# Kernel optimization log

Measured on AMD Instinct MI355X. Metric: run time of the kernel, lower is better.

## Reference

```python
import jax, jax.numpy as jnp
import numpy as np

N = 100000
E = 800000
IN_FEATS = 128
H_FEATS = 128
HEADS = 4
OUT = H_FEATS // HEADS  # 32
NEG_SLOPE = 0.2  # DGL GATConv default


def gat_conv(x, src, dst, W, attn_l, attn_r, bias):
    """DGL-style GATConv. x: [N, F_in] -> [N, HEADS, OUT]."""
    h = (x @ W).reshape(N, HEADS, OUT)                      # projected features
    el = jnp.sum(h * attn_l, axis=-1)                       # [N, H]
    er = jnp.sum(h * attn_r, axis=-1)                       # [N, H]
    e = jax.nn.leaky_relu(el[src] + er[dst], NEG_SLOPE)     # [E, H] edge logits
    # edge softmax over incoming edges of each dst node
    m = jax.ops.segment_max(e, dst, num_segments=N)          # [N, H]
    ex = jnp.exp(e - m[dst])                                 # [E, H]
    s = jax.ops.segment_sum(ex, dst, num_segments=N)         # [N, H]
    a = ex / s[dst]                                          # [E, H]
    msg = h[src] * a[:, :, None]                             # [E, H, OUT]
    out = jax.ops.segment_sum(msg, dst, num_segments=N)      # [N, H, OUT]
    return out + bias.reshape(1, HEADS, OUT)


def setup_inputs() -> dict:
    key = jax.random.key(0)
    ks = jax.random.split(key, 12)
    feat = jax.random.normal(ks[0], (N, IN_FEATS), dtype=jnp.float32)
    src = jax.random.randint(ks[1], (E,), 0, N)
    dst = jax.random.randint(ks[2], (E,), 0, N)
    s1 = 1.0 / np.sqrt(IN_FEATS)
    s2 = 1.0 / np.sqrt(H_FEATS)
    return {
        "feat": feat,
        "src": src,
        "dst": dst,
        "W1": jax.random.normal(ks[3], (IN_FEATS, HEADS * OUT), dtype=jnp.float32) * s1,
        "al1": jax.random.normal(ks[4], (HEADS, OUT), dtype=jnp.float32) * s2,
        "ar1": jax.random.normal(ks[5], (HEADS, OUT), dtype=jnp.float32) * s2,
        "b1": jnp.zeros((HEADS * OUT,), dtype=jnp.float32),
        "W2": jax.random.normal(ks[6], (H_FEATS, HEADS * OUT), dtype=jnp.float32) * s2,
        "al2": jax.random.normal(ks[7], (HEADS, OUT), dtype=jnp.float32) * s2,
        "ar2": jax.random.normal(ks[8], (HEADS, OUT), dtype=jnp.float32) * s2,
        "b2": jnp.zeros((HEADS * OUT,), dtype=jnp.float32),
    }


def reference(feat, src, dst, W1, al1, ar1, b1, W2, al2, ar2, b2):
    h = gat_conv(feat, src, dst, W1, al1, ar1, b1).reshape(N, H_FEATS)  # flatten(1)
    h = jax.nn.relu(h)
    h = gat_conv(h, src, dst, W2, al2, ar2, b2).mean(axis=1)            # mean over heads
    return h
```

## Files before the change

### kernel.cpp

```cpp
#include <hip/hip_runtime.h>
#include <math.h>

#define N_NODES 100000
#define N_EDGES 800000
#define NEG_SLOPE 0.2f

typedef __attribute__((ext_vector_type(8))) short short8;
typedef __attribute__((ext_vector_type(4))) float floatx4;

__device__ __forceinline__ float lrelu(float x) { return x > 0.f ? x : NEG_SLOPE * x; }

__device__ __forceinline__ unsigned bf16_rne(float f) {
    unsigned u = __float_as_uint(f);
    return (u + 0x7fffu + ((u >> 16) & 1u)) >> 16;
}
__device__ __forceinline__ unsigned bfpack(float lo, float hi) {
    return bf16_rne(lo) | (bf16_rne(hi) << 16);
}
__device__ __forceinline__ float bflo(unsigned p) { return __uint_as_float(p << 16); }
__device__ __forceinline__ float bfhi(unsigned p) { return __uint_as_float(p & 0xffff0000u); }

__global__ __launch_bounds__(256) void k_hist_wprep(const int* __restrict__ dst,
                                                    int* __restrict__ deg,
                                                    const float* __restrict__ W1,
                                                    const float* __restrict__ W2,
                                                    unsigned short* __restrict__ wt1,
                                                    unsigned short* __restrict__ wt2) {
    int b = blockIdx.x;
    if (b < 3125) {
        int e = b * 256 + threadIdx.x;
        if (e < N_EDGES) atomicAdd(&deg[dst[e]], 1);
    } else {
        int tid = (b - 3125) * 256 + threadIdx.x;
        const float* W = (tid < 16384) ? W1 : W2;
        unsigned short* wt = (tid < 16384) ? wt1 : wt2;
        int t = tid & 16383;
        int n = t >> 7, k = t & 127;
        wt[t] = (unsigned short)bf16_rne(W[k * 128 + n]);
    }
}

__global__ __launch_bounds__(256) void k_scan(const int* __restrict__ deg,
                                              int* __restrict__ rs,
                                              int* __restrict__ cursor,
                                              int* __restrict__ bsums,
                                              int* __restrict__ done) {
    __shared__ int sd[256];
    int tid = threadIdx.x, b = blockIdx.x;
    int base = b * 1024 + tid * 4;
    int v0 = (base + 0 < N_NODES) ? deg[base + 0] : 0;
    int v1 = (base + 1 < N_NODES) ? deg[base + 1] : 0;
    int v2 = (base + 2 < N_NODES) ? deg[base + 2] : 0;
    int v3 = (base + 3 < N_NODES) ? deg[base + 3] : 0;
    int t = v0 + v1 + v2 + v3;
    sd[tid] = t;
    __syncthreads();
    int incl = t;
    for (int off = 1; off < 256; off <<= 1) {
        int x = (tid >= off) ? sd[tid - off] : 0;
        __syncthreads();
        incl += x;
        sd[tid] = incl;
        __syncthreads();
    }
    int excl = incl - t;

    if (tid == 255) {
        atomicExch(&bsums[b], incl);
        __threadfence();
        atomicAdd(done, 1);
    }
    if (tid == 0) {
        while (atomicAdd(done, 0) < 98) { }
    }
    __syncthreads();

    int bv = (tid < b) ? atomicAdd(&bsums[tid], 0) : 0;
    __syncthreads();
    sd[tid] = bv;
    __syncthreads();
    for (int off = 128; off > 0; off >>= 1) {
        if (tid < off) sd[tid] += sd[tid + off];
        __syncthreads();
    }
    int boff = sd[0];

    int p0 = excl + boff;
    if (base + 0 < N_NODES) { rs[base + 0] = p0; cursor[base + 0] = p0; }
    if (base + 1 < N_NODES) { rs[base + 1] = p0 + v0; cursor[base + 1] = p0 + v0; }
    if (base + 2 < N_NODES) { rs[base + 2] = p0 + v0 + v1; cursor[base + 2] = p0 + v0 + v1; }
    if (base + 3 < N_NODES) { rs[base + 3] = p0 + v0 + v1 + v2; cursor[base + 3] = p0 + v0 + v1 + v2; }
    if (b == 0 && tid == 0) rs[N_NODES] = N_EDGES;
}

__global__ void k_scatter(const int* __restrict__ src, const int* __restrict__ dst,
                          int* __restrict__ cursor, int* __restrict__ csr_src) {
    int e = blockIdx.x * blockDim.x + threadIdx.x;
    if (e < N_EDGES) {
        int d = dst[e];
        int p = atomicAdd(&cursor[d], 1);
        csr_src[p] = src[e];
    }
}

__global__ __launch_bounds__(256) void k_gemm(const void* __restrict__ Xv,
                                              const unsigned short* __restrict__ wt,
                                              const float* __restrict__ al,
                                              const float* __restrict__ ar,
                                              unsigned* __restrict__ Hb,
                                              float* __restrict__ EL,
                                              float* __restrict__ ER,
                                              int src_bf16) {
    __shared__ unsigned short wsh[128 * 128];
    __shared__ unsigned short xsh[128 * 128];
    int tid = threadIdx.x;
    int w = tid >> 6, lane = tid & 63;
    int q = lane >> 4, nl = lane & 15;
    int base = blockIdx.x * 128;

    const uint4* wt4 = (const uint4*)wt;
    #pragma unroll
    for (int i = 0; i < 8; i++) {
        int idx = tid + i * 256;
        int rn = idx >> 4, c8 = idx & 15;
        int kc = c8 >> 2, qq = c8 & 3;
        int slot = rn * 128 + ((kc ^ ((rn >> 2) & 3)) * 4 + (qq ^ (rn & 3))) * 8;
        *(uint4*)&wsh[slot] = wt4[idx];
    }

    if (!src_bf16) {
        const float4* X4 = (const float4*)Xv;
        #pragma unroll
        for (int i = 0; i < 8; i++) {
            int idx = tid + i * 256;
            int rn = idx >> 4, c8 = idx & 15;
            int rr = base + rn; if (rr >= N_NODES) rr = N_NODES - 1;
            float4 a = X4[(size_t)rr * 32 + c8 * 2];
            float4 bb = X4[(size_t)rr * 32 + c8 * 2 + 1];
            int kc = c8 >> 2, qq = c8 & 3;
            int slot = rn * 128 + ((kc ^ ((rn >> 2) & 3)) * 4 + (qq ^ (rn & 3))) * 8;
            uint4 pk;
            pk.x = bfpack(a.x, a.y); pk.y = bfpack(a.z, a.w);
            pk.z = bfpack(bb.x, bb.y); pk.w = bfpack(bb.z, bb.w);
            *(uint4*)&xsh[slot] = pk;
        }
    } else {
        const uint4* Xb4 = (const uint4*)Xv;
        #pragma unroll
        for (int i = 0; i < 8; i++) {
            int idx = tid + i * 256;
            int rn = idx >> 4, c8 = idx & 15;
            int rr = base + rn; if (rr >= N_NODES) rr = N_NODES - 1;
            int kc = c8 >> 2, qq = c8 & 3;
            int slot = rn * 128 + ((kc ^ ((rn >> 2) & 3)) * 4 + (qq ^ (rn & 3))) * 8;
            *(uint4*)&xsh[slot] = Xb4[(size_t)rr * 16 + c8];
        }
    }

    __syncthreads();

    int sw_hi = (nl >> 2) & 3, sw_lo = nl & 3;

    short8 afr[2][4];
    #pragma unroll
    for (int rt = 0; rt < 2; rt++) {
        int r = w * 32 + rt * 16 + nl;
        #pragma unroll
        for (int kc = 0; kc < 4; kc++)
            afr[rt][kc] = *(const short8*)&xsh[r * 128 + ((kc ^ sw_hi) * 4 + (q ^ sw_lo)) * 8];
    }

    floatx4 acc[2][8];
    #pragma unroll
    for (int rt = 0; rt < 2; rt++)
        #pragma unroll
        for (int ct = 0; ct < 8; ct++)
            acc[rt][ct] = (floatx4){0.f, 0.f, 0.f, 0.f};

    #pragma unroll
    for (int ct = 0; ct < 8; ct++) {
        int rbase = (ct * 16 + nl) * 128;
        #pragma unroll
        for (int kc = 0; kc < 4; kc++) {
            short8 b = *(const short8*)&wsh[rbase + ((kc ^ sw_hi) * 4 + (q ^ sw_lo)) * 8];
            acc[0][ct] = __builtin_amdgcn_mfma_f32_16x16x32_bf16(afr[0][kc], b, acc[0][ct], 0, 0, 0);
            acc[1][ct] = __builtin_amdgcn_mfma_f32_16x16x32_bf16(afr[1][kc], b, acc[1][ct], 0, 0, 0);
        }
    }

    float all_[4], alh_[4], arl_[4], arh_[4];
    #pragma unroll
    for (int h = 0; h < 4; h++) {
        all_[h] = al[h * 32 + nl]; alh_[h] = al[h * 32 + 16 + nl];
        arl_[h] = ar[h * 32 + nl]; arh_[h] = ar[h * 32 + 16 + nl];
    }
    #pragma unroll
    for (int rt = 0; rt < 2; rt++) {
        #pragma unroll
        for (int r = 0; r < 4; r++) {
            int row = base + w * 32 + rt * 16 + q * 4 + r;
            bool valid = row < N_NODES;
            unsigned* hrow = Hb + (size_t)row * 64;
            #pragma unroll
            for (int ct = 0; ct < 8; ct++) {
                float vlo = acc[rt][ct][r];
                float vhi = __shfl_down(vlo, 1);
                if (valid && !(nl & 1)) hrow[ct * 8 + (nl >> 1)] = bfpack(vlo, vhi);
            }
            #pragma unroll
            for (int h = 0; h < 4; h++) {
                float pel = acc[rt][2 * h][r] * all_[h] + acc[rt][2 * h + 1][r] * alh_[h];
                float per = acc[rt][2 * h][r] * arl_[h] + acc[rt][2 * h + 1][r] * arh_[h];
                #pragma unroll
                for (int o = 1; o < 16; o <<= 1) {
                    pel += __shfl_xor(pel, o);
                    per += __shfl_xor(per, o);
                }
                if (valid && nl == 0) { EL[row * 4 + h] = pel; ER[row * 4 + h] = per; }
            }
        }
    }
}

__global__ __launch_bounds__(256) void k_gather(const int* __restrict__ rs,
                                                const int* __restrict__ csr_src,
                                                const float* __restrict__ EL,
                                                const float* __restrict__ ER,
                                                const unsigned* __restrict__ Hb,
                                                const float* __restrict__ bias,
                                                void* __restrict__ out,
                                                int final_layer) {
    int wid = (blockIdx.x * blockDim.x + threadIdx.x) >> 6;
    int lane = threadIdx.x & 63;
    int g = lane >> 4, l16 = lane & 15;
    int h = l16 >> 2;
    int n0 = wid * 4;
    if (n0 >= N_NODES) return;
    int nend = min(n0 + 4, N_NODES);

    float bv[8];
    #pragma unroll
    for (int c = 0; c < 8; c++) bv[c] = bias[l16 * 8 + c];

    for (int n = n0; n < nend; n++) {
        int s = rs[n], e = rs[n + 1];
        float erh = ER[n * 4 + h];
        float acc[8];
        #pragma unroll
        for (int c = 0; c < 8; c++) acc[c] = 0.f;
        float sa = 0.f;

        for (int j = s; j < e; j += 8) {
            int j0 = j + g, j1 = j + 4 + g;
            uint4 p0 = make_uint4(0, 0, 0, 0), p1 = make_uint4(0, 0, 0, 0);
            float w0 = 0.f, w1 = 0.f;
            if (j0 < e) {
                int s0 = csr_src[j0];
                p0 = *(const uint4*)(Hb + (size_t)s0 * 64 + l16 * 4);
                w0 = __expf(lrelu(EL[s0 * 4 + h] + erh));
            }
            if (j1 < e) {
                int s1 = csr_src[j1];
                p1 = *(const uint4*)(Hb + (size_t)s1 * 64 + l16 * 4);
                w1 = __expf(lrelu(EL[s1 * 4 + h] + erh));
            }
            sa += w0 + w1;
            acc[0] = fmaf(bflo(p0.x), w0, acc[0]); acc[1] = fmaf(bfhi(p0.x), w0, acc[1]);
            acc[2] = fmaf(bflo(p0.y), w0, acc[2]); acc[3] = fmaf(bfhi(p0.y), w0, acc[3]);
            acc[4] = fmaf(bflo(p0.z), w0, acc[4]); acc[5] = fmaf(bfhi(p0.z), w0, acc[5]);
            acc[6] = fmaf(bflo(p0.w), w0, acc[6]); acc[7] = fmaf(bfhi(p0.w), w0, acc[7]);
            acc[0] = fmaf(bflo(p1.x), w1, acc[0]); acc[1] = fmaf(bfhi(p1.x), w1, acc[1]);
            acc[2] = fmaf(bflo(p1.y), w1, acc[2]); acc[3] = fmaf(bfhi(p1.y), w1, acc[3]);
            acc[4] = fmaf(bflo(p1.z), w1, acc[4]); acc[5] = fmaf(bfhi(p1.z), w1, acc[5]);
            acc[6] = fmaf(bflo(p1.w), w1, acc[6]); acc[7] = fmaf(bfhi(p1.w), w1, acc[7]);
        }

        #pragma unroll
        for (int c = 0; c < 8; c++) {
            acc[c] += __shfl_xor(acc[c], 16);
            acc[c] += __shfl_xor(acc[c], 32);
        }
        sa += __shfl_xor(sa, 16);
        sa += __shfl_xor(sa, 32);
        float inv = (e > s) ? 1.f / sa : 0.f;

        float r[8];
        #pragma unroll
        for (int c = 0; c < 8; c++) r[c] = acc[c] * inv + bv[c];

        if (!final_layer) {
            if (g == 0) {
                uint4 pk;
                pk.x = bfpack(fmaxf(r[0], 0.f), fmaxf(r[1], 0.f));
                pk.y = bfpack(fmaxf(r[2], 0.f), fmaxf(r[3], 0.f));
                pk.z = bfpack(fmaxf(r[4], 0.f), fmaxf(r[5], 0.f));
                pk.w = bfpack(fmaxf(r[6], 0.f), fmaxf(r[7], 0.f));
                *(uint4*)((unsigned*)out + (size_t)n * 64 + l16 * 4) = pk;
            }
        } else {
            #pragma unroll
            for (int c = 0; c < 8; c++) {
                r[c] += __shfl_xor(r[c], 4);
                r[c] += __shfl_xor(r[c], 8);
            }
            if (g == 0 && l16 < 4) {
                float* po = (float*)out + (size_t)n * 32 + l16 * 8;
                *(float4*)po = make_float4(0.25f * r[0], 0.25f * r[1], 0.25f * r[2], 0.25f * r[3]);
                *(float4*)(po + 4) = make_float4(0.25f * r[4], 0.25f * r[5], 0.25f * r[6], 0.25f * r[7]);
            }
        }
    }
}

extern "C" void kernel_launch(void* const* d_in, const int* in_sizes, int n_in,
                              void* d_out, int out_size, void* d_ws, size_t ws_size,
                              hipStream_t stream) {
    const float* feat = (const float*)d_in[0];
    const int* src = (const int*)d_in[1];
    const int* dst = (const int*)d_in[2];
    const float* W1 = (const float*)d_in[3];
    const float* al1 = (const float*)d_in[4];
    const float* ar1 = (const float*)d_in[5];
    const float* b1 = (const float*)d_in[6];
    const float* W2 = (const float*)d_in[7];
    const float* al2 = (const float*)d_in[8];
    const float* ar2 = (const float*)d_in[9];
    const float* b2 = (const float*)d_in[10];
    float* out = (float*)d_out;

    char* ws = (char*)d_ws;
    size_t off = 0;
    auto alloc = [&](size_t bytes) {
        void* p = ws + off;
        off += (bytes + 255) & ~(size_t)255;
        return p;
    };
    int* deg = (int*)alloc((size_t)N_NODES * 4);
    int* done = (int*)alloc(256);
    int* rs = (int*)alloc(((size_t)N_NODES + 1) * 4);
    int* cursor = (int*)alloc((size_t)N_NODES * 4);
    int* bsums = (int*)alloc(128 * 4);
    int* csr_src = (int*)alloc((size_t)N_EDGES * 4);
    unsigned* Hb = (unsigned*)alloc((size_t)N_NODES * 64 * 4);
    float* el = (float*)alloc((size_t)N_NODES * 4 * 4);
    float* er = (float*)alloc((size_t)N_NODES * 4 * 4);
    unsigned* out1b = (unsigned*)alloc((size_t)N_NODES * 64 * 4);
    unsigned short* wt1 = (unsigned short*)alloc(128 * 128 * 2);
    unsigned short* wt2 = (unsigned short*)alloc(128 * 128 * 2);

    size_t zbytes = (size_t)((char*)done - (char*)deg) + 256;
    hipMemsetAsync(deg, 0, zbytes, stream);

    k_hist_wprep<<<3125 + 128, 256, 0, stream>>>(dst, deg, W1, W2, wt1, wt2);
    k_scan<<<98, 256, 0, stream>>>(deg, rs, cursor, bsums, done);
    k_scatter<<<(N_EDGES + 255) / 256, 256, 0, stream>>>(src, dst, cursor, csr_src);

    int gemm_blocks = (N_NODES + 127) / 128;
    int gat_blocks = (N_NODES + 15) / 16;

    k_gemm<<<gemm_blocks, 256, 0, stream>>>(feat, wt1, al1, ar1, Hb, el, er, 0);
    k_gather<<<gat_blocks, 256, 0, stream>>>(rs, csr_src, el, er, Hb, b1, out1b, 0);
    k_gemm<<<gemm_blocks, 256, 0, stream>>>(out1b, wt2, al2, ar2, Hb, el, er, 1);
    k_gather<<<gat_blocks, 256, 0, stream>>>(rs, csr_src, el, er, Hb, b2, out, 1);
}
```

Before: 344.8 us.

## Fuse CSR build into persistent kernel and fold attention vectors into GEMM

Merges the histogram, scan and scatter kernels into one persistent 98-block kernel that uses software grid barriers, which removes separate launches and the large memset. Weight prep and a new precomputation of W·attn_l/attn_r, stored as extra bf16 columns, run on side blocks of the same launch. The GEMM loads its A fragments straight from global memory instead of staging them in LDS, and computes el/er with extra MFMAs instead of shuffle reductions. The costs are reduced edge-pass parallelism (only 98 blocks do the atomics), a reliance on all 98 blocks being co-resident, and el/er computed with bf16-rounded attention weights.

```diff
diff --git a/kernel.cpp b/kernel.cpp
--- a/kernel.cpp
+++ b/kernel.cpp
@@ -4,6 +4,8 @@
 #define N_NODES 100000
 #define N_EDGES 800000
 #define NEG_SLOPE 0.2f
+#define NB_CSR 98
+#define NT_CSR (NB_CSR * 256)
 
 typedef __attribute__((ext_vector_type(8))) short short8;
 typedef __attribute__((ext_vector_type(4))) float floatx4;
@@ -20,38 +22,76 @@
 __device__ __forceinline__ float bflo(unsigned p) { return __uint_as_float(p << 16); }
 __device__ __forceinline__ float bfhi(unsigned p) { return __uint_as_float(p & 0xffff0000u); }
 
-__global__ __launch_bounds__(256) void k_hist_wprep(const int* __restrict__ dst,
-                                                    int* __restrict__ deg,
-                                                    const float* __restrict__ W1,
-                                                    const float* __restrict__ W2,
-                                                    unsigned short* __restrict__ wt1,
-                                                    unsigned short* __restrict__ wt2) {
-    int b = blockIdx.x;
-    if (b < 3125) {
-        int e = b * 256 + threadIdx.x;
-        if (e < N_EDGES) atomicAdd(&deg[dst[e]], 1);
-    } else {
-        int tid = (b - 3125) * 256 + threadIdx.x;
-        const float* W = (tid < 16384) ? W1 : W2;
-        unsigned short* wt = (tid < 16384) ? wt1 : wt2;
-        int t = tid & 16383;
-        int n = t >> 7, k = t & 127;
-        wt[t] = (unsigned short)bf16_rne(W[k * 128 + n]);
-    }
-}
-
-__global__ __launch_bounds__(256) void k_scan(const int* __restrict__ deg,
-                                              int* __restrict__ rs,
-                                              int* __restrict__ cursor,
-                                              int* __restrict__ bsums,
-                                              int* __restrict__ done) {
+__device__ __forceinline__ void gbar(int* ctr) {
+    __syncthreads();
+    if (threadIdx.x == 0) {
+        __threadfence();
+        atomicAdd(ctr, 1);
+        while (atomicAdd(ctr, 0) < NB_CSR) { }
+    }
+    __syncthreads();
+}
+
+__global__ __launch_bounds__(256) void k_pre(const int* __restrict__ src,
+                                             const int* __restrict__ dst,
+                                             int* __restrict__ deg,
+                                             int* __restrict__ rs,
+                                             int* __restrict__ cursor,
+                                             int* __restrict__ bsums,
+                                             int* __restrict__ done,
+                                             int* __restrict__ csr_src,
+                                             const float* __restrict__ W1,
+                                             const float* __restrict__ al1,
+                                             const float* __restrict__ ar1,
+                                             const float* __restrict__ W2,
+                                             const float* __restrict__ al2,
+                                             const float* __restrict__ ar2,
+                                             unsigned short* __restrict__ wt1,
+                                             unsigned short* __restrict__ wt2,
+                                             unsigned short* __restrict__ et1,
+                                             unsigned short* __restrict__ et2) {
+    int b = blockIdx.x, tid = threadIdx.x;
+    if (b >= NB_CSR) {
+        int wb = b - NB_CSR;
+        if (wb < 128) {
+            int t2 = wb * 256 + tid;
+            const float* W = (t2 < 16384) ? W1 : W2;
+            unsigned short* wt = (t2 < 16384) ? wt1 : wt2;
+            int t = t2 & 16383;
+            int n = t >> 7, k = t & 127;
+            wt[t] = (unsigned short)bf16_rne(W[k * 128 + n]);
+        } else {
+            const float* W = (wb == 128) ? W1 : W2;
+            const float* al = (wb == 128) ? al1 : al2;
+            const float* ar = (wb == 128) ? ar1 : ar2;
+            unsigned short* et = (wb == 128) ? et1 : et2;
+            for (int o = tid * 8; o < tid * 8 + 8; o++) {
+                int n = o >> 7, k = o & 127;
+                float sacc = 0.f;
+                if (n < 8) {
+                    const float* a = (n < 4) ? al : ar;
+                    int hh = n & 3;
+                    #pragma unroll 8
+                    for (int c = 0; c < 32; c++)
+                        sacc += W[k * 128 + hh * 32 + c] * a[hh * 32 + c];
+                }
+                et[n * 128 + k] = (unsigned short)bf16_rne(sacc);
+            }
+        }
+        return;
+    }
+
+    int gtid = b * 256 + tid;
+    for (int i = gtid; i < N_NODES; i += NT_CSR) deg[i] = 0;
+    gbar(&done[0]);
+    for (int e = gtid; e < N_EDGES; e += NT_CSR) atomicAdd(&deg[dst[e]], 1);
+    gbar(&done[1]);
     __shared__ int sd[256];
-    int tid = threadIdx.x, b = blockIdx.x;
     int base = b * 1024 + tid * 4;
-    int v0 = (base + 0 < N_NODES) ? deg[base + 0] : 0;
-    int v1 = (base + 1 < N_NODES) ? deg[base + 1] : 0;
-    int v2 = (base + 2 < N_NODES) ? deg[base + 2] : 0;
-    int v3 = (base + 3 < N_NODES) ? deg[base + 3] : 0;
+    int v0 = (base + 0 < N_NODES) ? atomicAdd(&deg[base + 0], 0) : 0;
+    int v1 = (base + 1 < N_NODES) ? atomicAdd(&deg[base + 1], 0) : 0;
+    int v2 = (base + 2 < N_NODES) ? atomicAdd(&deg[base + 2], 0) : 0;
+    int v3 = (base + 3 < N_NODES) ? atomicAdd(&deg[base + 3], 0) : 0;
     int t = v0 + v1 + v2 + v3;
     sd[tid] = t;
     __syncthreads();
@@ -68,10 +108,10 @@
     if (tid == 255) {
         atomicExch(&bsums[b], incl);
         __threadfence();
-        atomicAdd(done, 1);
+        atomicAdd(&done[2], 1);
     }
     if (tid == 0) {
-        while (atomicAdd(done, 0) < 98) { }
+        while (atomicAdd(&done[2], 0) < NB_CSR) { }
     }
     __syncthreads();
 
@@ -91,12 +131,8 @@
     if (base + 2 < N_NODES) { rs[base + 2] = p0 + v0 + v1; cursor[base + 2] = p0 + v0 + v1; }
     if (base + 3 < N_NODES) { rs[base + 3] = p0 + v0 + v1 + v2; cursor[base + 3] = p0 + v0 + v1 + v2; }
     if (b == 0 && tid == 0) rs[N_NODES] = N_EDGES;
-}
-
-__global__ void k_scatter(const int* __restrict__ src, const int* __restrict__ dst,
-                          int* __restrict__ cursor, int* __restrict__ csr_src) {
-    int e = blockIdx.x * blockDim.x + threadIdx.x;
-    if (e < N_EDGES) {
+    gbar(&done[3]);
+    for (int e = gtid; e < N_EDGES; e += NT_CSR) {
         int d = dst[e];
         int p = atomicAdd(&cursor[d], 1);
         csr_src[p] = src[e];
@@ -105,14 +141,13 @@
 
 __global__ __launch_bounds__(256) void k_gemm(const void* __restrict__ Xv,
                                               const unsigned short* __restrict__ wt,
-                                              const float* __restrict__ al,
-                                              const float* __restrict__ ar,
+                                              const unsigned short* __restrict__ et,
                                               unsigned* __restrict__ Hb,
                                               float* __restrict__ EL,
                                               float* __restrict__ ER,
                                               int src_bf16) {
     __shared__ unsigned short wsh[128 * 128];
-    __shared__ unsigned short xsh[128 * 128];
+    __shared__ unsigned short esh[16 * 136];
     int tid = threadIdx.x;
     int w = tid >> 6, lane = tid & 63;
     int q = lane >> 4, nl = lane & 15;
@@ -127,56 +162,55 @@
         int slot = rn * 128 + ((kc ^ ((rn >> 2) & 3)) * 4 + (qq ^ (rn & 3))) * 8;
         *(uint4*)&wsh[slot] = wt4[idx];
     }
-
+    {
+        const uint4* et4 = (const uint4*)et;
+        int rn = tid >> 4, c8 = tid & 15;
+        *(uint4*)&esh[rn * 136 + c8 * 8] = et4[tid];
+    }
+
+    short8 afr[2][4];
+    int row0 = base + w * 32 + nl;
     if (!src_bf16) {
         const float4* X4 = (const float4*)Xv;
         #pragma unroll
-        for (int i = 0; i < 8; i++) {
-            int idx = tid + i * 256;
-            int rn = idx >> 4, c8 = idx & 15;
-            int rr = base + rn; if (rr >= N_NODES) rr = N_NODES - 1;
-            float4 a = X4[(size_t)rr * 32 + c8 * 2];
-            float4 bb = X4[(size_t)rr * 32 + c8 * 2 + 1];
-            int kc = c8 >> 2, qq = c8 & 3;
-            int slot = rn * 128 + ((kc ^ ((rn >> 2) & 3)) * 4 + (qq ^ (rn & 3))) * 8;
-            uint4 pk;
-            pk.x = bfpack(a.x, a.y); pk.y = bfpack(a.z, a.w);
-            pk.z = bfpack(bb.x, bb.y); pk.w = bfpack(bb.z, bb.w);
-            *(uint4*)&xsh[slot] = pk;
+        for (int rt = 0; rt < 2; rt++) {
+            int rr = row0 + rt * 16; if (rr > N_NODES - 1) rr = N_NODES - 1;
+            const float4* px = X4 + (size_t)rr * 32 + q * 2;
+            #pragma unroll
+            for (int kc = 0; kc < 4; kc++) {
+                float4 u = px[kc * 8], v = px[kc * 8 + 1];
+                short8 f;
+                f[0] = (short)bf16_rne(u.x); f[1] = (short)bf16_rne(u.y);
+                f[2] = (short)bf16_rne(u.z); f[3] = (short)bf16_rne(u.w);
+                f[4] = (short)bf16_rne(v.x); f[5] = (short)bf16_rne(v.y);
+                f[6] = (short)bf16_rne(v.z); f[7] = (short)bf16_rne(v.w);
+                afr[rt][kc] = f;
+            }
         }
     } else {
-        const uint4* Xb4 = (const uint4*)Xv;
-        #pragma unroll
-        for (int i = 0; i < 8; i++) {
-            int idx = tid + i * 256;
-            int rn = idx >> 4, c8 = idx & 15;
-            int rr = base + rn; if (rr >= N_NODES) rr = N_NODES - 1;
-            int kc = c8 >> 2, qq = c8 & 3;
-            int slot = rn * 128 + ((kc ^ ((rn >> 2) & 3)) * 4 + (qq ^ (rn & 3))) * 8;
-            *(uint4*)&xsh[slot] = Xb4[(size_t)rr * 16 + c8];
-        }
-    }
-
-    __syncthreads();
-
-    int sw_hi = (nl >> 2) & 3, sw_lo = nl & 3;
-
-    short8 afr[2][4];
+        const unsigned short* Xb = (const unsigned short*)Xv;
+        #pragma unroll
+        for (int rt = 0; rt < 2; rt++) {
+            int rr = row0 + rt * 16; if (rr > N_NODES - 1) rr = N_NODES - 1;
+            #pragma unroll
+            for (int kc = 0; kc < 4; kc++)
+                afr[rt][kc] = *(const short8*)(Xb + (size_t)rr * 128 + kc * 32 + q * 8);
+        }
+    }
+
+    floatx4 acc[2][8];
+    floatx4 acc_e[2];
     #pragma unroll
     for (int rt = 0; rt < 2; rt++) {
-        int r = w * 32 + rt * 16 + nl;
-        #pragma unroll
-        for (int kc = 0; kc < 4; kc++)
-            afr[rt][kc] = *(const short8*)&xsh[r * 128 + ((kc ^ sw_hi) * 4 + (q ^ sw_lo)) * 8];
-    }
-
-    floatx4 acc[2][8];
-    #pragma unroll
-    for (int rt = 0; rt < 2; rt++)
+        acc_e[rt] = (floatx4){0.f, 0.f, 0.f, 0.f};
         #pragma unroll
         for (int ct = 0; ct < 8; ct++)
             acc[rt][ct] = (floatx4){0.f, 0.f, 0.f, 0.f};
-
+    }
+
+    __syncthreads();
+
+    int sw_hi = (nl >> 2) & 3, sw_lo = nl & 3;
     #pragma unroll
     for (int ct = 0; ct < 8; ct++) {
         int rbase = (ct * 16 + nl) * 128;
@@ -187,13 +221,13 @@
             acc[1][ct] = __builtin_amdgcn_mfma_f32_16x16x32_bf16(afr[1][kc], b, acc[1][ct], 0, 0, 0);
         }
     }
-
-    float all_[4], alh_[4], arl_[4], arh_[4];
-    #pragma unroll
-    for (int h = 0; h < 4; h++) {
-        all_[h] = al[h * 32 + nl]; alh_[h] = al[h * 32 + 16 + nl];
-        arl_[h] = ar[h * 32 + nl]; arh_[h] = ar[h * 32 + 16 + nl];
-    }
+    #pragma unroll
+    for (int kc = 0; kc < 4; kc++) {
+        short8 e8 = *(const short8*)&esh[nl * 136 + (kc * 4 + q) * 8];
+        acc_e[0] = __builtin_amdgcn_mfma_f32_16x16x32_bf16(afr[0][kc], e8, acc_e[0], 0, 0, 0);
+        acc_e[1] = __builtin_amdgcn_mfma_f32_16x16x32_bf16(afr[1][kc], e8, acc_e[1], 0, 0, 0);
+    }
+
     #pragma unroll
     for (int rt = 0; rt < 2; rt++) {
         #pragma unroll
@@ -207,16 +241,10 @@
                 float vhi = __shfl_down(vlo, 1);
                 if (valid && !(nl & 1)) hrow[ct * 8 + (nl >> 1)] = bfpack(vlo, vhi);
             }
-            #pragma unroll
-            for (int h = 0; h < 4; h++) {
-                float pel = acc[rt][2 * h][r] * all_[h] + acc[rt][2 * h + 1][r] * alh_[h];
-                float per = acc[rt][2 * h][r] * arl_[h] + acc[rt][2 * h + 1][r] * arh_[h];
-                #pragma unroll
-                for (int o = 1; o < 16; o <<= 1) {
-                    pel += __shfl_xor(pel, o);
-                    per += __shfl_xor(per, o);
-                }
-                if (valid && nl == 0) { EL[row * 4 + h] = pel; ER[row * 4 + h] = per; }
+            if (valid && nl < 8) {
+                float v = acc_e[rt][r];
+                if (nl < 4) EL[row * 4 + nl] = v;
+                else        ER[row * 4 + (nl & 3)] = v;
             }
         }
     }
@@ -335,8 +363,8 @@
         off += (bytes + 255) & ~(size_t)255;
         return p;
     };
+    int* done = (int*)alloc(256);
     int* deg = (int*)alloc((size_t)N_NODES * 4);
-    int* done = (int*)alloc(256);
     int* rs = (int*)alloc(((size_t)N_NODES + 1) * 4);
     int* cursor = (int*)alloc((size_t)N_NODES * 4);
     int* bsums = (int*)alloc(128 * 4);
@@ -347,19 +375,20 @@
     unsigned* out1b = (unsigned*)alloc((size_t)N_NODES * 64 * 4);
     unsigned short* wt1 = (unsigned short*)alloc(128 * 128 * 2);
     unsigned short* wt2 = (unsigned short*)alloc(128 * 128 * 2);
-
-    size_t zbytes = (size_t)((char*)done - (char*)deg) + 256;
-    hipMemsetAsync(deg, 0, zbytes, stream);
-
-    k_hist_wprep<<<3125 + 128, 256, 0, stream>>>(dst, deg, W1, W2, wt1, wt2);
-    k_scan<<<98, 256, 0, stream>>>(deg, rs, cursor, bsums, done);
-    k_scatter<<<(N_EDGES + 255) / 256, 256, 0, stream>>>(src, dst, cursor, csr_src);
+    unsigned short* et1 = (unsigned short*)alloc(16 * 128 * 2);
+    unsigned short* et2 = (unsigned short*)alloc(16 * 128 * 2);
+
+    hipMemsetAsync(done, 0, 256, stream);
+
+    k_pre<<<NB_CSR + 128 + 2, 256, 0, stream>>>(src, dst, deg, rs, cursor, bsums, done,
+                                                csr_src, W1, al1, ar1, W2, al2, ar2,
+                                                wt1, wt2, et1, et2);
 
     int gemm_blocks = (N_NODES + 127) / 128;
     int gat_blocks = (N_NODES + 15) / 16;
 
-    k_gemm<<<gemm_blocks, 256, 0, stream>>>(feat, wt1, al1, ar1, Hb, el, er, 0);
+    k_gemm<<<gemm_blocks, 256, 0, stream>>>(feat, wt1, et1, Hb, el, er, 0);
     k_gather<<<gat_blocks, 256, 0, stream>>>(rs, csr_src, el, er, Hb, b1, out1b, 0);
-    k_gemm<<<gemm_blocks, 256, 0, stream>>>(out1b, wt2, al2, ar2, Hb, el, er, 1);
+    k_gemm<<<gemm_blocks, 256, 0, stream>>>(out1b, wt2, et2, Hb, el, er, 1);
     k_gather<<<gat_blocks, 256, 0, stream>>>(rs, csr_src, el, er, Hb, b2, out, 1);
 }
```

Result: faster. 330.8 us (-4.1%).
